# Kernel tuning notes

Measured on AMD Instinct MI355X. Metric: run time of the kernel, lower is better.

## Reference

```python
import jax, jax.numpy as jnp
import numpy as np

# Static architecture sizes (see shape_source)
B, H, W, NCH = 64, 64, 64, 3
K = 2                     # kernel at every stage
D = 20                    # bond_dim == virtual_dim
OUT = 10                  # output_dim
P1 = (H // K) * (W // K)          # 1024 patches, stage 1
P2 = P1 // (K * K)                # 256 patches, stage 2
P3 = P2 // (K * K)                # 64 patches, stage 3
FP = 2 * K * K                    # feature_dim per stage = 2*ker^2 = 8
FF = 2 * D                        # feature_dim of final MPS = 2*virtual_dim


def _unfold(x, k):
    # torch: x.unfold(2,k,k).unfold(3,k,k).reshape(b, k*k, -1, C)
    b, C, Hh, Ww = x.shape
    v = x.reshape(b, C, Hh // k, k, Ww // k, k).transpose(0, 1, 2, 4, 3, 5)
    return v.reshape(b, k * k, -1, C)   # [b, k^2, P, C] (raw reshape, faithful)


def _batchnorm(y, g, bb, eps=1e-5):
    # BatchNorm1d(C) on [b, C, L], training mode (batch stats), affine
    mu = jnp.mean(y, axis=(0, 2), keepdims=True)
    var = jnp.var(y, axis=(0, 2), keepdims=True)
    return g[None, :, None] * (y - mu) * jax.lax.rsqrt(var + eps) + bb[None, :, None]


def _mps(x, cores, label, alpha, omega):
    # Batched tensor-train contraction over independent per-patch MPS modules.
    # x:     [b, Fraw, P, S]  (S sites per MPS, P independent MPS modules)
    # cores: [P, S, 2*Fraw, D, D], label: [O, D, D], alpha/omega: [D]
    phi = jnp.concatenate([x, 1.0 - x], axis=1)              # [b, F, P, S]
    M = jnp.einsum('bfps,psfij->spbij', phi, cores)          # per-site transfer mats
    def step(c, m):
        return jnp.einsum('pbij,pbjk->pbik', c, m), None
    eye = jnp.broadcast_to(jnp.eye(cores.shape[-1], dtype=x.dtype), M.shape[1:])
    tot, _ = jax.lax.scan(step, eye, M)                      # [P, b, D, D]
    return jnp.einsum('i,pbij,ojk,k->bpo', alpha, tot, label, omega)  # [b, P, O]


def _cores(key, P, S, F):
    # near-identity init; sum_f phi_f = Fraw = F/2, so scale eye by 2/F
    return (jnp.eye(D, dtype=jnp.float32) * (2.0 / F)
            + 0.01 * jax.random.normal(key, (P, S, F, D, D), jnp.float32))


def setup_inputs() -> dict:
    ks = jax.random.split(jax.random.key(0), 12)
    one, zero = jnp.ones((D,), jnp.float32), jnp.zeros
    return {
        'x': jax.random.normal(ks[0], (B, NCH, H, W), jnp.float32),
        'cores1': _cores(ks[1], P1, NCH, FP),
        'label1': 0.1 * jax.random.normal(ks[2], (D, D, D), jnp.float32),
        'alpha1': one, 'omega1': one,
        'g1': jnp.ones((P1,), jnp.float32), 'b1': zero((P1,), jnp.float32),
        'cores2': _cores(ks[3], P2, D, FP),
        'label2': 0.1 * jax.random.normal(ks[4], (D, D, D), jnp.float32),
        'alpha2': one, 'omega2': one,
        'g2': jnp.ones((P2,), jnp.float32), 'b2': zero((P2,), jnp.float32),
        'cores3': _cores(ks[5], P3, D, FP),
        'label3': 0.1 * jax.random.normal(ks[6], (D, D, D), jnp.float32),
        'alpha3': one, 'omega3': one,
        'g3': jnp.ones((P3,), jnp.float32), 'b3': zero((P3,), jnp.float32),
        'coresF': _cores(ks[7], 1, P3, FF),
        'labelF': 0.1 * jax.random.normal(ks[8], (OUT, D, D), jnp.float32),
        'alphaF': one, 'omegaF': one,
    }


def reference(x, cores1, label1, alpha1, omega1, g1, b1,
              cores2, label2, alpha2, omega2, g2, b2,
              cores3, label3, alpha3, omega3, g3, b3,
              coresF, labelF, alphaF, omegaF):
    b = x.shape[0]
    u = _unfold(x, K)                              # [b, 4, P1, 3]
    y = _mps(u, cores1, label1, alpha1, omega1)    # [b, P1, D]
    y = _batchnorm(y, g1, b1).reshape(b, D, H // K, W // K)   # raw view, faithful
    u = _unfold(y, K)                              # [b, 4, P2, D]
    y = _mps(u, cores2, label2, alpha2, omega2)    # [b, P2, D]
    y = _batchnorm(y, g2, b2).reshape(b, D, H // (K * K), W // (K * K))
    u = _unfold(y, K)                              # [b, 4, P3, D]
    y = _mps(u, cores3, label3, alpha3, omega3)    # [b, P3, D]
    y = _batchnorm(y, g3, b3)
    y = jnp.transpose(y, (0, 2, 1))                # [b, D, P3]
    out = _mps(y[:, :, None, :], coresF, labelF, alphaF, omegaF)[:, 0, :]
    return out                                     # [b, OUT]
```

## Files before the change

### kernel.cpp

```cpp
#include <hip/hip_runtime.h>
#include <hip/hip_bf16.h>

typedef __attribute__((ext_vector_type(4))) float f32x4;
typedef __attribute__((ext_vector_type(8))) short s16x8;

static __device__ __forceinline__ short f2bf(float x) {
  __hip_bfloat16 h = __float2bfloat16(x);
  return *reinterpret_cast<short*>(&h);
}

template<int STAGE>
__global__ __launch_bounds__(256)
void k_mps(const float* __restrict__ xsrc, const float* __restrict__ ysrc,
           const float* __restrict__ cores, const float* __restrict__ alpha,
           const float* __restrict__ label, const float* __restrict__ omega,
           const float* __restrict__ gam, const float* __restrict__ bet,
           float* __restrict__ yout) {
  constexpr int S = (STAGE == 1) ? 3 : 20;
  __shared__ __align__(16) float u4[S][64][4];
  __shared__ __align__(16) short Cl[2][32][168];
  __shared__ __align__(16) float vls[64][36];
  __shared__ float Lw_l[400];
  __shared__ float redA[4], redB[4], stats[2];

  const int p = blockIdx.x, t = threadIdx.x;
  const int b = t & 63, q = t >> 6;
  const int m = b & 15, quad = b >> 4;
  const int bl = q * 16 + m;

  const bool two = (t < 144);
  const float* cbase = cores + (size_t)p * S * 3200;

  float p0A[8], p0B[8], p1A[8], p1B[8];
#pragma unroll
  for (int g = 0; g < 8; ++g) p0A[g] = cbase[g * 400 + t];
  if (two) {
#pragma unroll
    for (int g = 0; g < 8; ++g) p0B[g] = cbase[g * 400 + 256 + t];
  }

  for (int e = t; e < 400; e += 256) {
    int o = e / 20, j = e % 20;
    float a = 0.f;
#pragma unroll
    for (int k = 0; k < 20; ++k) a = fmaf(label[o * 400 + j * 20 + k], omega[k], a);
    Lw_l[e] = a;
  }

  {
    int* cz = (int*)&Cl[0][0][0];
    for (int i = t; i < 5376; i += 256) cz[i] = 0;
    for (int i = t; i < 64 * 36; i += 256) {
      int col = i % 36;
      vls[i / 36][col] = (col < 20) ? alpha[col] : 0.f;
    }
  }

  for (int k = 0; k < S; ++k) {
    float val;
    if (STAGE == 1) {
      int L = q * 3072 + p * 3 + k;
      int c = L >> 12, r = L & 4095;
      int hh = 2 * (r >> 7) + ((r >> 1) & 1);
      int ww = 2 * ((r >> 2) & 31) + (r & 1);
      val = xsrc[(b * 3 + c) * 4096 + hh * 64 + ww];
    } else if (STAGE == 2) {
      int L = q * 5120 + p * 20 + k;
      int c = L >> 10, r = L & 1023;
      int f = c * 1024 + (2 * (r >> 6) + ((r >> 1) & 1)) * 32
                        + (2 * ((r >> 2) & 15) + (r & 1));
      val = ysrc[f * 64 + b];
    } else {
      int L = q * 1280 + p * 20 + k;
      int c = L >> 8, r = L & 255;
      int f = c * 256 + (2 * (r >> 5) + ((r >> 1) & 1)) * 16
                       + (2 * ((r >> 2) & 7) + (r & 1));
      val = ysrc[f * 64 + b];
    }
    u4[k][b][q] = val;
  }

  auto writeC = [&](int buf, int e, const float* r) {
    int i = e / 20, j = e % 20;
    Cl[buf][j][      i] = f2bf(r[0] - r[4]);
    Cl[buf][j][ 32 + i] = f2bf(r[1] - r[5]);
    Cl[buf][j][ 64 + i] = f2bf(r[2] - r[6]);
    Cl[buf][j][ 96 + i] = f2bf(r[3] - r[7]);
    float cs = r[4] + r[5] + r[6] + r[7];
    if (i == j) cs -= 1.f;
    Cl[buf][j][128 + i] = f2bf(cs);
  };
  auto loadSite = [&](int s, float (&rA)[8], float (&rB)[8]) {
    const float* cs = cbase + (size_t)s * 3200;
#pragma unroll
    for (int g = 0; g < 8; ++g) rA[g] = cs[g * 400 + t];
    if (two) {
#pragma unroll
      for (int g = 0; g < 8; ++g) rB[g] = cs[g * 400 + 256 + t];
    }
  };

  writeC(0, t, p0A);
  if (two) writeC(0, t + 256, p0B);
  if (S > 1) loadSite(1, p0A, p0B);
  if (S > 2) loadSite(2, p1A, p1B);
  __syncthreads();

  auto site_step = [&](int s, int cur, float (&rA)[8], float (&rB)[8]) {
    const float4 uu = *(const float4*)&u4[s][bl][0];
    const float4 va = *(const float4*)&vls[bl][quad * 8];
    const float4 vb = *(const float4*)&vls[bl][quad * 8 + 4];
    const float vv[8] = {va.x, va.y, va.z, va.w, vb.x, vb.y, vb.z, vb.w};
    const float um[5] = {uu.x, uu.y, uu.z, uu.w, 1.f};

    f32x4 acc0 = {0.f, 0.f, 0.f, 0.f};
    f32x4 acc1 = {0.f, 0.f, 0.f, 0.f};
#pragma unroll
    for (int kt = 0; kt < 5; ++kt) {
      s16x8 aF;
#pragma unroll
      for (int j2 = 0; j2 < 8; ++j2) aF[j2] = f2bf(vv[j2] * um[kt]);
      const s16x8 bF0 = *(const s16x8*)&Cl[cur][m][kt * 32 + quad * 8];
      const s16x8 bF1 = *(const s16x8*)&Cl[cur][m + 16][kt * 32 + quad * 8];
      acc0 = __builtin_amdgcn_mfma_f32_16x16x32_bf16(aF, bF0, acc0, 0, 0, 0);
      acc1 = __builtin_amdgcn_mfma_f32_16x16x32_bf16(aF, bF1, acc1, 0, 0, 0);
    }

    if (s + 1 < S) {
      writeC(cur ^ 1, t, rA);
      if (two) writeC(cur ^ 1, t + 256, rB);
      if (s + 3 < S) loadSite(s + 3, rA, rB);
    }

#pragma unroll
    for (int r = 0; r < 4; ++r) vls[q * 16 + quad * 4 + r][m] += acc0[r];
    if (m < 4) {
#pragma unroll
      for (int r = 0; r < 4; ++r) vls[q * 16 + quad * 4 + r][m + 16] += acc1[r];
    }
    __syncthreads();
  };

  for (int s = 0; s < S; s += 2) {
    site_step(s, 0, p0A, p0B);
    if (s + 1 < S) site_step(s + 1, 1, p1A, p1B);
  }

  float vf[20];
  {
    const float4 v0 = *(const float4*)&vls[b][0];
    const float4 v1 = *(const float4*)&vls[b][4];
    const float4 v2 = *(const float4*)&vls[b][8];
    const float4 v3 = *(const float4*)&vls[b][12];
    const float4 v4 = *(const float4*)&vls[b][16];
    vf[0]=v0.x; vf[1]=v0.y; vf[2]=v0.z; vf[3]=v0.w;
    vf[4]=v1.x; vf[5]=v1.y; vf[6]=v1.z; vf[7]=v1.w;
    vf[8]=v2.x; vf[9]=v2.y; vf[10]=v2.z; vf[11]=v2.w;
    vf[12]=v3.x; vf[13]=v3.y; vf[14]=v3.z; vf[15]=v3.w;
    vf[16]=v4.x; vf[17]=v4.y; vf[18]=v4.z; vf[19]=v4.w;
  }
  float yo[5];
  float s1 = 0.f, s2 = 0.f;
#pragma unroll
  for (int jj = 0; jj < 5; ++jj) {
    int o = q * 5 + jj;
    float a = 0.f;
#pragma unroll
    for (int j = 0; j < 20; ++j) a = fmaf(vf[j], Lw_l[o * 20 + j], a);
    yo[jj] = a; s1 += a; s2 += a * a;
  }
#pragma unroll
  for (int off = 32; off > 0; off >>= 1) {
    s1 += __shfl_down(s1, off); s2 += __shfl_down(s2, off);
  }
  if (b == 0) { redA[q] = s1; redB[q] = s2; }
  __syncthreads();
  if (t == 0) {
    float S1 = redA[0] + redA[1] + redA[2] + redA[3];
    float S2 = redB[0] + redB[1] + redB[2] + redB[3];
    float mu = S1 * (1.f / 1280.f);
    float var = S2 * (1.f / 1280.f) - mu * mu;
    if (var < 0.f) var = 0.f;
    stats[0] = mu; stats[1] = var;
  }
  __syncthreads();
  float mu = stats[0], var = stats[1];
  float scale = gam[p] / sqrtf(var + 1e-5f);
  float shift = bet[p] - mu * scale;
#pragma unroll
  for (int jj = 0; jj < 5; ++jj) {
    int o = q * 5 + jj;
    yout[(p * 20 + o) * 64 + b] = fmaf(yo[jj], scale, shift);
  }
}


__global__ __launch_bounds__(256)
void k_mbuild(const float* __restrict__ yn3, const float* __restrict__ coresF,
              float* __restrict__ Mmat) {
  __shared__ float ybn[64][20];
  const int s = blockIdx.x >> 2, bq = blockIdx.x & 3;
  const int t = threadIdx.x;
  for (int i = t; i < 1280; i += 256) ybn[i & 63][i >> 6] = yn3[(size_t)s * 1280 + i];
  __syncthreads();
  const float* cfp = coresF + (size_t)s * 16000;
  for (int e = t; e < 400; e += 256) {
    float dlt[20]; float hsum = 0.f;
#pragma unroll
    for (int g = 0; g < 20; ++g) {
      float lo = cfp[g * 400 + e], hi = cfp[(g + 20) * 400 + e];
      dlt[g] = lo - hi; hsum += hi;
    }
    for (int bb = bq * 16; bb < bq * 16 + 16; ++bb) {
      const float4* yb = (const float4*)ybn[bb];
      float yy[20];
      *(float4*)&yy[0]  = yb[0]; *(float4*)&yy[4]  = yb[1];
      *(float4*)&yy[8]  = yb[2]; *(float4*)&yy[12] = yb[3];
      *(float4*)&yy[16] = yb[4];
      float a = hsum;
#pragma unroll
      for (int g = 0; g < 20; ++g) a = fmaf(yy[g], dlt[g], a);
      Mmat[((size_t)s * 64 + bb) * 400 + e] = a;
    }
  }
}

__global__ __launch_bounds__(256)
void k_chain(const float* __restrict__ Mmat, const float* __restrict__ alphaF,
             const float* __restrict__ labelF, const float* __restrict__ omegaF,
             float* __restrict__ out) {
  const int b = blockIdx.x, t = threadIdx.x;
  __shared__ float Pb[2][400];
  __shared__ float Mb[2][400];
  __shared__ float LwF[200];
  __shared__ float va[20];

  if (t < 200) {
    int o = t / 20, j = t % 20;
    float a = 0.f;
#pragma unroll
    for (int k = 0; k < 20; ++k) a = fmaf(labelF[o * 400 + j * 20 + k], omegaF[k], a);
    LwF[t] = a;
  }
  for (int e = t; e < 400; e += 256) Pb[0][e] = Mmat[(size_t)b * 400 + e];
  float r0 = Mmat[(size_t)(64 + b) * 400 + t];
  float r1 = (t < 144) ? Mmat[(size_t)(64 + b) * 400 + 256 + t] : 0.f;
  __syncthreads();

  int cur = 0;
  for (int s = 1; s < 64; ++s) {
    Mb[s & 1][t] = r0;
    if (t < 144) Mb[s & 1][256 + t] = r1;
    __syncthreads();
    if (s + 1 < 64) {
      r0 = Mmat[(size_t)((s + 1) * 64 + b) * 400 + t];
      if (t < 144) r1 = Mmat[(size_t)((s + 1) * 64 + b) * 400 + 256 + t];
    }
    for (int e = t; e < 400; e += 256) {
      int i = e / 20, j = e - (e / 20) * 20;
      float a = 0.f;
#pragma unroll
      for (int k = 0; k < 20; ++k)
        a = fmaf(Pb[cur][i * 20 + k], Mb[s & 1][k * 20 + j], a);
      Pb[cur ^ 1][e] = a;
    }
    cur ^= 1;
    __syncthreads();
  }
  if (t < 20) {
    float a = 0.f;
#pragma unroll
    for (int i = 0; i < 20; ++i) a = fmaf(alphaF[i], Pb[cur][i * 20 + t], a);
    va[t] = a;
  }
  __syncthreads();
  if (t < 10) {
    float a = 0.f;
#pragma unroll
    for (int j = 0; j < 20; ++j) a = fmaf(va[j], LwF[t * 20 + j], a);
    out[b * 10 + t] = a;
  }
}

extern "C" void kernel_launch(void* const* d_in, const int* in_sizes, int n_in,
                              void* d_out, int out_size, void* d_ws, size_t ws_size,
                              hipStream_t stream) {
  const float* x      = (const float*)d_in[0];
  const float* cores1 = (const float*)d_in[1];
  const float* label1 = (const float*)d_in[2];
  const float* alpha1 = (const float*)d_in[3];
  const float* omega1 = (const float*)d_in[4];
  const float* g1     = (const float*)d_in[5];
  const float* b1     = (const float*)d_in[6];
  const float* cores2 = (const float*)d_in[7];
  const float* label2 = (const float*)d_in[8];
  const float* alpha2 = (const float*)d_in[9];
  const float* omega2 = (const float*)d_in[10];
  const float* g2     = (const float*)d_in[11];
  const float* b2     = (const float*)d_in[12];
  const float* cores3 = (const float*)d_in[13];
  const float* label3 = (const float*)d_in[14];
  const float* alpha3 = (const float*)d_in[15];
  const float* omega3 = (const float*)d_in[16];
  const float* g3     = (const float*)d_in[17];
  const float* b3     = (const float*)d_in[18];
  const float* coresF = (const float*)d_in[19];
  const float* labelF = (const float*)d_in[20];
  const float* alphaF = (const float*)d_in[21];
  const float* omegaF = (const float*)d_in[22];

  float* ws   = (float*)d_ws;
  float* yn1  = ws;
  float* yn2  = yn1 + 1310720;
  float* yn3  = yn2 + 327680;
  float* Mmat = yn3 + 81920;
  float* out  = (float*)d_out;

  k_mps<1><<<1024, 256, 0, stream>>>(x, nullptr, cores1, alpha1, label1, omega1, g1, b1, yn1);
  k_mps<2><<<256, 256, 0, stream>>>(nullptr, yn1, cores2, alpha2, label2, omega2, g2, b2, yn2);
  k_mps<3><<<64, 256, 0, stream>>>(nullptr, yn2, cores3, alpha3, label3, omega3, g3, b3, yn3);
  k_mbuild<<<256, 256, 0, stream>>>(yn3, coresF, Mmat);
  k_chain<<<64, 256, 0, stream>>>(Mmat, alphaF, labelF, omegaF, out);
}
```

Baseline: 282.4 us.

## Split final MPS chain into per-wave chunks and carry MPS accumulators in registers

The final 64-site chain is split into 8 chunks of 8 sites. Each wave multiplies its own chunk with wave-local LDS sync instead of block barriers, and the 8 chunk products are then combined serially. In the per-stage MPS kernel the MFMA accumulators are seeded from register copies of the state vector, so the read-modify-write into shared memory becomes a plain store. This aims to shorten the serial 63-step chain latency at the cost of more LDS, wave-level sync via inline waitcnt, and a different floating-point association order.

```diff
diff --git a/kernel.cpp b/kernel.cpp
--- a/kernel.cpp
+++ b/kernel.cpp
@@ -7,6 +7,11 @@
 static __device__ __forceinline__ short f2bf(float x) {
   __hip_bfloat16 h = __float2bfloat16(x);
   return *reinterpret_cast<short*>(&h);
+}
+
+static __device__ __forceinline__ void wave_lgkm0() {
+  asm volatile("s_waitcnt lgkmcnt(0)" ::: "memory");
+  __builtin_amdgcn_sched_barrier(0);
 }
 
 template<int STAGE>
@@ -54,6 +59,14 @@
       int col = i % 36;
       vls[i / 36][col] = (col < 20) ? alpha[col] : 0.f;
     }
+  }
+
+  float vr0[4], vr1[4];
+  {
+    float a0 = alpha[m];
+    float a1 = (m < 4) ? alpha[m + 16] : 0.f;
+#pragma unroll
+    for (int r = 0; r < 4; ++r) { vr0[r] = a0; vr1[r] = a1; }
   }
 
   for (int k = 0; k < S; ++k) {
@@ -113,8 +126,9 @@
     const float vv[8] = {va.x, va.y, va.z, va.w, vb.x, vb.y, vb.z, vb.w};
     const float um[5] = {uu.x, uu.y, uu.z, uu.w, 1.f};
 
-    f32x4 acc0 = {0.f, 0.f, 0.f, 0.f};
-    f32x4 acc1 = {0.f, 0.f, 0.f, 0.f};
+    f32x4 acc0, acc1;
+#pragma unroll
+    for (int r = 0; r < 4; ++r) { acc0[r] = vr0[r]; acc1[r] = vr1[r]; }
 #pragma unroll
     for (int kt = 0; kt < 5; ++kt) {
       s16x8 aF;
@@ -133,10 +147,12 @@
     }
 
 #pragma unroll
-    for (int r = 0; r < 4; ++r) vls[q * 16 + quad * 4 + r][m] += acc0[r];
+    for (int r = 0; r < 4; ++r) { vr0[r] = acc0[r]; vr1[r] = acc1[r]; }
+#pragma unroll
+    for (int r = 0; r < 4; ++r) vls[q * 16 + quad * 4 + r][m] = acc0[r];
     if (m < 4) {
 #pragma unroll
-      for (int r = 0; r < 4; ++r) vls[q * 16 + quad * 4 + r][m + 16] += acc1[r];
+      for (int r = 0; r < 4; ++r) vls[q * 16 + quad * 4 + r][m + 16] = acc1[r];
     }
     __syncthreads();
   };
@@ -194,7 +210,6 @@
   }
 }
 
-
 __global__ __launch_bounds__(256)
 void k_mbuild(const float* __restrict__ yn3, const float* __restrict__ coresF,
               float* __restrict__ Mmat) {
@@ -225,13 +240,15 @@
   }
 }
 
-__global__ __launch_bounds__(256)
-void k_chain(const float* __restrict__ Mmat, const float* __restrict__ alphaF,
-             const float* __restrict__ labelF, const float* __restrict__ omegaF,
-             float* __restrict__ out) {
-  const int b = blockIdx.x, t = threadIdx.x;
-  __shared__ float Pb[2][400];
-  __shared__ float Mb[2][400];
+__global__ __launch_bounds__(512)
+void k_fin(const float* __restrict__ Mmat, const float* __restrict__ alphaF,
+           const float* __restrict__ labelF, const float* __restrict__ omegaF,
+           float* __restrict__ out) {
+  const int bb = blockIdx.x, t = threadIdx.x;
+  const int w = t >> 6, l = t & 63;
+  __shared__ float Pw[8][2][400];
+  __shared__ float Mw[8][400];
+  __shared__ float chunkP[8][400];
   __shared__ float LwF[200];
   __shared__ float va[20];
 
@@ -242,35 +259,77 @@
     for (int k = 0; k < 20; ++k) a = fmaf(labelF[o * 400 + j * 20 + k], omegaF[k], a);
     LwF[t] = a;
   }
-  for (int e = t; e < 400; e += 256) Pb[0][e] = Mmat[(size_t)b * 400 + e];
-  float r0 = Mmat[(size_t)(64 + b) * 400 + t];
-  float r1 = (t < 144) ? Mmat[(size_t)(64 + b) * 400 + 256 + t] : 0.f;
-  __syncthreads();
-
+
+  float pre[7];
+  {
+    const size_t b0 = ((size_t)(w * 8) * 64 + bb) * 400;
+#pragma unroll
+    for (int it = 0; it < 7; ++it) {
+      int e = l + 64 * it;
+      pre[it] = (e < 400) ? Mmat[b0 + e] : 0.f;
+    }
+#pragma unroll
+    for (int it = 0; it < 7; ++it) {
+      int e = l + 64 * it;
+      if (e < 400) Pw[w][0][e] = pre[it];
+    }
+  }
   int cur = 0;
-  for (int s = 1; s < 64; ++s) {
-    Mb[s & 1][t] = r0;
-    if (t < 144) Mb[s & 1][256 + t] = r1;
+  for (int ls = 1; ls < 8; ++ls) {
+    const size_t mb = ((size_t)(w * 8 + ls) * 64 + bb) * 400;
+#pragma unroll
+    for (int it = 0; it < 7; ++it) {
+      int e = l + 64 * it;
+      if (e < 400) pre[it] = Mmat[mb + e];
+    }
+#pragma unroll
+    for (int it = 0; it < 7; ++it) {
+      int e = l + 64 * it;
+      if (e < 400) Mw[w][e] = pre[it];
+    }
+    wave_lgkm0();
+    if (l < 60) {
+      const int j = l % 20, ii = l / 20;
+      float mc[20];
+#pragma unroll
+      for (int k = 0; k < 20; ++k) mc[k] = Mw[w][k * 20 + j];
+      for (int i = ii; i < 20; i += 3) {
+        float a = 0.f;
+#pragma unroll
+        for (int k = 0; k < 20; ++k) a = fmaf(Pw[w][cur][i * 20 + k], mc[k], a);
+        Pw[w][cur ^ 1][i * 20 + j] = a;
+      }
+    }
+    wave_lgkm0();
+    cur ^= 1;
+  }
+#pragma unroll
+  for (int it = 0; it < 7; ++it) {
+    int e = l + 64 * it;
+    if (e < 400) chunkP[w][e] = Pw[w][cur][e];
+  }
+  __syncthreads();
+
+  float* T0 = &Mw[0][0];
+  float* T1 = &Mw[1][0];
+  if (t < 400) T0[t] = chunkP[0][t];
+  __syncthreads();
+  float* Tc = T0; float* Tn = T1;
+  for (int c = 1; c < 8; ++c) {
+    if (t < 400) {
+      int i = t / 20, j = t - (t / 20) * 20;
+      float a = 0.f;
+#pragma unroll
+      for (int k = 0; k < 20; ++k) a = fmaf(Tc[i * 20 + k], chunkP[c][k * 20 + j], a);
+      Tn[t] = a;
+    }
     __syncthreads();
-    if (s + 1 < 64) {
-      r0 = Mmat[(size_t)((s + 1) * 64 + b) * 400 + t];
-      if (t < 144) r1 = Mmat[(size_t)((s + 1) * 64 + b) * 400 + 256 + t];
-    }
-    for (int e = t; e < 400; e += 256) {
-      int i = e / 20, j = e - (e / 20) * 20;
-      float a = 0.f;
-#pragma unroll
-      for (int k = 0; k < 20; ++k)
-        a = fmaf(Pb[cur][i * 20 + k], Mb[s & 1][k * 20 + j], a);
-      Pb[cur ^ 1][e] = a;
-    }
-    cur ^= 1;
-    __syncthreads();
+    float* tmp = Tc; Tc = Tn; Tn = tmp;
   }
   if (t < 20) {
     float a = 0.f;
 #pragma unroll
-    for (int i = 0; i < 20; ++i) a = fmaf(alphaF[i], Pb[cur][i * 20 + t], a);
+    for (int i = 0; i < 20; ++i) a = fmaf(alphaF[i], Tc[i * 20 + t], a);
     va[t] = a;
   }
   __syncthreads();
@@ -278,7 +337,7 @@
     float a = 0.f;
 #pragma unroll
     for (int j = 0; j < 20; ++j) a = fmaf(va[j], LwF[t * 20 + j], a);
-    out[b * 10 + t] = a;
+    out[bb * 10 + t] = a;
   }
 }
 
@@ -320,5 +379,5 @@
   k_mps<2><<<256, 256, 0, stream>>>(nullptr, yn1, cores2, alpha2, label2, omega2, g2, b2, yn2);
   k_mps<3><<<64, 256, 0, stream>>>(nullptr, yn2, cores3, alpha3, label3, omega3, g3, b3, yn3);
   k_mbuild<<<256, 256, 0, stream>>>(yn3, coresF, Mmat);
-  k_chain<<<64, 256, 0, stream>>>(Mmat, alphaF, labelF, omegaF, out);
-}
+  k_fin<<<64, 512, 0, stream>>>(Mmat, alphaF, labelF, omegaF, out);
+}
```

Result: faster. 254.2 us (-10.0%).
